# Performance work log

Measured on AMD Instinct MI355X. Metric: run time of the kernel, lower is better.

## Reference

```python
import jax, jax.numpy as jnp
import numpy as np

B, M, C = 8, 1024, 768


def setup_inputs() -> dict:
    key = jax.random.key(0)
    ks = jax.random.split(key, 10)
    s = 0.02
    return {
        "layout_x": jax.random.normal(ks[0], (B, M, C), jnp.float32),
        "text_x": jax.random.normal(ks[1], (B, M, C), jnp.float32),
        "mask": jax.random.randint(ks[2], (B, M), 0, 2).astype(jnp.float32),
        "Wqkv": jax.random.normal(ks[3], (C, 3 * C), jnp.float32) * s,
        "bqkv": jnp.zeros((3 * C,), jnp.float32),
        "Wq": jax.random.normal(ks[4], (C, C), jnp.float32) * s,
        "bq": jnp.zeros((C,), jnp.float32),
        "Wkv": jax.random.normal(ks[5], (C, 2 * C), jnp.float32) * s,
        "bkv": jnp.zeros((2 * C,), jnp.float32),
        "Wffn": jax.random.normal(ks[6], (C, C), jnp.float32) * s,
        "bffn": jnp.zeros((C,), jnp.float32),
    }


def _masked_attn(q, k, v, pair_mask, scale):
    # pair_mask: [B,M,M] True where valid (mask_i * mask_j != 0)
    scores = jnp.einsum("bmd,bnd->bmn", q, k) * scale  # [B,M,M]
    scores = jnp.where(pair_mask, scores, jnp.float32(-10000.0))
    attn = jax.nn.softmax(scores, axis=-1)
    return jnp.einsum("bmn,bnd->bmd", attn, v)


def reference(layout_x, text_x, mask, Wqkv, bqkv, Wq, bq, Wkv, bkv, Wffn, bffn):
    dim = layout_x.shape[-1]
    scale = dim ** (-0.5)
    # mask repeated over C then mask@mask.T / C  ==  outer product of 1D masks
    pair = (mask[:, :, None] * mask[:, None, :]) != 0  # [B,M,M] bool, True=keep

    # self-attention on layout_x
    qkv = layout_x @ Wqkv + bqkv  # [B,M,3C]
    q, k, v = jnp.split(qkv, 3, axis=-1)
    layout_o = _masked_attn(q, k, v, pair, scale)

    # cross-attention: q from layout output, k/v from text_x
    cq = layout_o @ Wq + bq
    kv = text_x @ Wkv + bkv  # [B,M,2C]
    ck, cv = jnp.split(kv, 2, axis=-1)
    merge = _masked_attn(cq, ck, cv, pair, scale)

    return merge @ Wffn + bffn
```

## Files before the change

kernel.cpp:

```cpp
#include <hip/hip_runtime.h>
#include <math.h>

#define BDIM 8
#define MDIM 1024
#define CDIM 768
#define ROWS (BDIM * MDIM)

typedef __attribute__((ext_vector_type(8))) short short8;
typedef __attribute__((ext_vector_type(8))) unsigned short ushort8;
typedef __attribute__((ext_vector_type(4))) float f32x4;

#define MFMA16(a, b, c) __builtin_amdgcn_mfma_f32_16x16x32_bf16((a), (b), (c), 0, 0, 0)

__device__ __forceinline__ unsigned short f2bf(float f) {
  unsigned u = __float_as_uint(f);
  return (unsigned short)((u + 0x7FFFu + ((u >> 16) & 1u)) >> 16);
}

__global__ __launch_bounds__(256) void convert_bf16(
    const float* __restrict__ src, unsigned short* __restrict__ dst, int n) {
  const int i = (blockIdx.x * 256 + threadIdx.x) * 8;
  if (i >= n) return;
  const float4 a = *(const float4*)(src + i);
  const float4 b = *(const float4*)(src + i + 4);
  ushort8 o;
  o[0] = f2bf(a.x); o[1] = f2bf(a.y); o[2] = f2bf(a.z); o[3] = f2bf(a.w);
  o[4] = f2bf(b.x); o[5] = f2bf(b.y); o[6] = f2bf(b.z); o[7] = f2bf(b.w);
  *(ushort8*)(dst + i) = o;
}

__global__ __launch_bounds__(256) void transpose_w(
    const float* __restrict__ W, int N, unsigned short* __restrict__ Wt) {
  __shared__ unsigned short t[32][33];
  const int tx = threadIdx.x, ty = threadIdx.y;
  const int n0 = blockIdx.x * 32, k0 = blockIdx.y * 32;
#pragma unroll
  for (int i = 0; i < 4; ++i)
    t[ty + i * 8][tx] = f2bf(W[(size_t)(k0 + ty + i * 8) * N + n0 + tx]);
  __syncthreads();
#pragma unroll
  for (int i = 0; i < 4; ++i)
    Wt[(size_t)(n0 + ty + i * 8) * CDIM + k0 + tx] = t[tx][ty + i * 8];
}

__global__ __launch_bounds__(256) void transpose_bf16(
    const unsigned short* __restrict__ src, int ld,
    unsigned short* __restrict__ dst) {
  __shared__ unsigned short t[32][33];
  const int tx = threadIdx.x, ty = threadIdx.y;
  const int n0 = blockIdx.x * 32, d0 = blockIdx.y * 32, b = blockIdx.z;
#pragma unroll
  for (int i = 0; i < 4; ++i) {
    const int n = n0 + ty + i * 8;
    t[ty + i * 8][tx] = src[(size_t)(b * MDIM + n) * ld + d0 + tx];
  }
  __syncthreads();
  unsigned short* db = dst + (size_t)b * CDIM * MDIM;
#pragma unroll
  for (int i = 0; i < 4; ++i) {
    const int d = d0 + ty + i * 8;
    db[(size_t)d * MDIM + n0 + tx] = t[tx][ty + i * 8];
  }
}

__device__ __forceinline__ void stage_tile(
    const unsigned short* __restrict__ g, int ld, int k0,
    unsigned short* lds, int wave, int lane) {
  const int gchunk = (lane & 3) ^ ((lane >> 3) & 3);
#pragma unroll
  for (int j = 0; j < 2; ++j) {
    const int grp = wave * 2 + j;
    const unsigned short* gp =
        g + (size_t)(grp * 16 + (lane >> 2)) * ld + k0 + gchunk * 8;
    __builtin_amdgcn_global_load_lds(
        (const __attribute__((address_space(1))) unsigned int*)gp,
        (__attribute__((address_space(3))) unsigned int*)(lds + grp * 512),
        16, 0, 0);
  }
}

__device__ __forceinline__ void mfma_loop(
    const unsigned short* __restrict__ A, int lda,
    const unsigned short* __restrict__ Bt, int ldb, int K,
    unsigned short* As, unsigned short* Bs, f32x4 acc[4][4],
    int wave, int lane) {
  const int wx = wave & 1, wy = wave >> 1;
  const int quad = lane >> 4, l16 = lane & 15;
  const int sq = (quad ^ ((l16 >> 1) & 3)) * 8;
  for (int k0 = 0; k0 < K; k0 += 32) {
    stage_tile(A, lda, k0, As, wave, lane);
    stage_tile(Bt, ldb, k0, Bs, wave, lane);
    __syncthreads();
    short8 afr[4], bfr[4];
#pragma unroll
    for (int mt = 0; mt < 4; ++mt)
      afr[mt] = *(const short8*)&As[(wy * 64 + mt * 16 + l16) * 32 + sq];
#pragma unroll
    for (int nt = 0; nt < 4; ++nt)
      bfr[nt] = *(const short8*)&Bs[(wx * 64 + nt * 16 + l16) * 32 + sq];
#pragma unroll
    for (int mt = 0; mt < 4; ++mt)
#pragma unroll
      for (int nt = 0; nt < 4; ++nt)
        acc[mt][nt] = MFMA16(afr[mt], bfr[nt], acc[mt][nt]);
    __syncthreads();
  }
}

template <bool BF16OUT>
__global__ __launch_bounds__(256, 3) void gemm_mfma(
    const unsigned short* __restrict__ A, const unsigned short* __restrict__ Bt,
    const float* __restrict__ bias, void* __restrict__ Yv) {
  __shared__ __align__(16) unsigned short As[128 * 32];
  __shared__ __align__(16) unsigned short Bs[128 * 32];
  const int c0 = blockIdx.x * 128;
  const int m0 = blockIdx.y * 128;
  const int tid = threadIdx.x;
  const int wave = tid >> 6, lane = tid & 63;
  const int wx = wave & 1, wy = wave >> 1;
  const int quad = lane >> 4, l16 = lane & 15;

  const f32x4 vzero = {0.f, 0.f, 0.f, 0.f};
  f32x4 acc[4][4];
#pragma unroll
  for (int mt = 0; mt < 4; ++mt)
#pragma unroll
    for (int nt = 0; nt < 4; ++nt) acc[mt][nt] = vzero;

  mfma_loop(A + (size_t)m0 * CDIM, CDIM, Bt + (size_t)c0 * CDIM, CDIM, CDIM,
            As, Bs, acc, wave, lane);

  const int slice = c0 / 768;
  const size_t sbase = (size_t)slice * ROWS * 768;
#pragma unroll
  for (int mt = 0; mt < 4; ++mt)
#pragma unroll
    for (int nt = 0; nt < 4; ++nt) {
      const int gcol = c0 + wx * 64 + nt * 16 + l16;
      const int lcol = gcol - slice * 768;
      const float bv = bias[gcol];
#pragma unroll
      for (int rg = 0; rg < 4; ++rg) {
        const int row = m0 + wy * 64 + mt * 16 + quad * 4 + rg;
        const float v = acc[mt][nt][rg] + bv;
        if (BF16OUT)
          ((unsigned short*)Yv)[sbase + (size_t)row * 768 + lcol] = f2bf(v);
        else
          ((float*)Yv)[sbase + (size_t)row * 768 + lcol] = v;
      }
    }
}

__global__ __launch_bounds__(256, 3) void gemm_qk(
    const unsigned short* __restrict__ Qb, const unsigned short* __restrict__ Kb,
    const float* __restrict__ mask, unsigned short* __restrict__ S, float scale) {
  __shared__ __align__(16) unsigned short As[128 * 32];
  __shared__ __align__(16) unsigned short Bs[128 * 32];
  const int c0 = blockIdx.x * 128;
  const int m0 = blockIdx.y * 128;
  const int b = blockIdx.z;
  const int tid = threadIdx.x;
  const int wave = tid >> 6, lane = tid & 63;
  const int wx = wave & 1, wy = wave >> 1;
  const int quad = lane >> 4, l16 = lane & 15;

  const f32x4 vzero = {0.f, 0.f, 0.f, 0.f};
  f32x4 acc[4][4];
#pragma unroll
  for (int mt = 0; mt < 4; ++mt)
#pragma unroll
    for (int nt = 0; nt < 4; ++nt) acc[mt][nt] = vzero;

  mfma_loop(Qb + ((size_t)b * MDIM + m0) * CDIM, CDIM,
            Kb + ((size_t)b * MDIM + c0) * CDIM, CDIM, CDIM,
            As, Bs, acc, wave, lane);

  const float* maskb = mask + b * MDIM;
  float mrow[4][4];
#pragma unroll
  for (int mt = 0; mt < 4; ++mt)
#pragma unroll
    for (int rg = 0; rg < 4; ++rg)
      mrow[mt][rg] = maskb[m0 + wy * 64 + mt * 16 + quad * 4 + rg];
  unsigned short* Sb = S + (size_t)b * MDIM * MDIM;
#pragma unroll
  for (int nt = 0; nt < 4; ++nt) {
    const int col = c0 + wx * 64 + nt * 16 + l16;
    const float mcol = maskb[col];
#pragma unroll
    for (int mt = 0; mt < 4; ++mt)
#pragma unroll
      for (int rg = 0; rg < 4; ++rg) {
        const int row = m0 + wy * 64 + mt * 16 + quad * 4 + rg;
        const float sv =
            (mrow[mt][rg] * mcol != 0.f) ? acc[mt][nt][rg] * scale : -10000.0f;
        Sb[(size_t)row * MDIM + col] = f2bf(sv);
      }
  }
}

__global__ __launch_bounds__(256) void softmax_row(unsigned short* __restrict__ S) {
  __shared__ float red[2][4];
  unsigned short* p = S + (size_t)blockIdx.x * MDIM;
  const int t = threadIdx.x;
  const int wave = t >> 6, lane = t & 63;
  const uint2 u = *(const uint2*)(p + t * 4);
  const float v0 = __uint_as_float((u.x & 0xFFFFu) << 16);
  const float v1 = __uint_as_float(u.x & 0xFFFF0000u);
  const float v2 = __uint_as_float((u.y & 0xFFFFu) << 16);
  const float v3 = __uint_as_float(u.y & 0xFFFF0000u);
  float mx = fmaxf(fmaxf(v0, v1), fmaxf(v2, v3));
  for (int off = 1; off < 64; off <<= 1) mx = fmaxf(mx, __shfl_xor(mx, off, 64));
  if (lane == 0) red[0][wave] = mx;
  __syncthreads();
  mx = fmaxf(fmaxf(red[0][0], red[0][1]), fmaxf(red[0][2], red[0][3]));
  const float e0 = __expf(v0 - mx), e1 = __expf(v1 - mx);
  const float e2 = __expf(v2 - mx), e3 = __expf(v3 - mx);
  float s = e0 + e1 + e2 + e3;
  for (int off = 1; off < 64; off <<= 1) s += __shfl_xor(s, off, 64);
  if (lane == 0) red[1][wave] = s;
  __syncthreads();
  const float inv = 1.f / (red[1][0] + red[1][1] + red[1][2] + red[1][3]);
  uint2 o;
  o.x = (unsigned)f2bf(e0 * inv) | ((unsigned)f2bf(e1 * inv) << 16);
  o.y = (unsigned)f2bf(e2 * inv) | ((unsigned)f2bf(e3 * inv) << 16);
  *(uint2*)(p + t * 4) = o;
}

__global__ __launch_bounds__(256, 3) void attn_pv(
    const unsigned short* __restrict__ P, const unsigned short* __restrict__ vT,
    unsigned short* __restrict__ O) {
  __shared__ __align__(16) unsigned short As[128 * 32];
  __shared__ __align__(16) unsigned short Bs[128 * 32];
  const int c0 = blockIdx.x * 128;
  const int m0 = blockIdx.y * 128;
  const int b = blockIdx.z;
  const int tid = threadIdx.x;
  const int wave = tid >> 6, lane = tid & 63;
  const int wx = wave & 1, wy = wave >> 1;
  const int quad = lane >> 4, l16 = lane & 15;

  const f32x4 vzero = {0.f, 0.f, 0.f, 0.f};
  f32x4 acc[4][4];
#pragma unroll
  for (int mt = 0; mt < 4; ++mt)
#pragma unroll
    for (int nt = 0; nt < 4; ++nt) acc[mt][nt] = vzero;

  mfma_loop(P + ((size_t)b * MDIM + m0) * MDIM, MDIM,
            vT + ((size_t)b * CDIM + c0) * MDIM, MDIM, MDIM,
            As, Bs, acc, wave, lane);

#pragma unroll
  for (int mt = 0; mt < 4; ++mt)
#pragma unroll
    for (int nt = 0; nt < 4; ++nt)
#pragma unroll
      for (int rg = 0; rg < 4; ++rg) {
        const int row = m0 + wy * 64 + mt * 16 + quad * 4 + rg;
        const int col = c0 + wx * 64 + nt * 16 + l16;
        O[(size_t)(b * MDIM + row) * CDIM + col] = f2bf(acc[mt][nt][rg]);
      }
}

extern "C" void kernel_launch(void* const* d_in, const int* in_sizes, int n_in,
                              void* d_out, int out_size, void* d_ws, size_t ws_size,
                              hipStream_t stream) {
  const float* layout_x = (const float*)d_in[0];
  const float* text_x   = (const float*)d_in[1];
  const float* maskp    = (const float*)d_in[2];
  const float* Wqkv     = (const float*)d_in[3];
  const float* bqkv     = (const float*)d_in[4];
  const float* Wq       = (const float*)d_in[5];
  const float* bq       = (const float*)d_in[6];
  const float* Wkv      = (const float*)d_in[7];
  const float* bkv      = (const float*)d_in[8];
  const float* Wffn     = (const float*)d_in[9];
  const float* bffn     = (const float*)d_in[10];
  float* out = (float*)d_out;
  char* ws = (char*)d_ws;

  const float scale = 1.0f / sqrtf((float)CDIM);

  unsigned short* xlb    = (unsigned short*)(ws);
  unsigned short* xtb    = (unsigned short*)(ws + 12582912);
  unsigned short* Wqkv_t = (unsigned short*)(ws + 25165824);
  unsigned short* Wq_t   = (unsigned short*)(ws + 28704768);
  unsigned short* Wkv_t  = (unsigned short*)(ws + 29884416);
  unsigned short* Wffn_t = (unsigned short*)(ws + 32243712);
  unsigned short* Qb     = (unsigned short*)(ws + 33423360);
  unsigned short* Kb     = (unsigned short*)(ws + 46006272);
  unsigned short* Vb     = (unsigned short*)(ws + 58589184);
  unsigned short* vT     = (unsigned short*)(ws + 71172096);
  unsigned short* S      = (unsigned short*)(ws + 83755008);
  unsigned short* attn1  = xlb;
  unsigned short* cqb    = Vb;
  unsigned short* Kc     = Qb;
  unsigned short* Vc     = Kb;

  convert_bf16<<<ROWS * CDIM / 2048, 256, 0, stream>>>(layout_x, xlb, ROWS * CDIM);
  convert_bf16<<<ROWS * CDIM / 2048, 256, 0, stream>>>(text_x, xtb, ROWS * CDIM);
  transpose_w<<<dim3(72, 24), dim3(32, 8), 0, stream>>>(Wqkv, 2304, Wqkv_t);
  transpose_w<<<dim3(24, 24), dim3(32, 8), 0, stream>>>(Wq, 768, Wq_t);
  transpose_w<<<dim3(48, 24), dim3(32, 8), 0, stream>>>(Wkv, 1536, Wkv_t);
  transpose_w<<<dim3(24, 24), dim3(32, 8), 0, stream>>>(Wffn, 768, Wffn_t);

  gemm_mfma<true><<<dim3(18, 64), 256, 0, stream>>>(xlb, Wqkv_t, bqkv, Qb);
  transpose_bf16<<<dim3(32, 24, BDIM), dim3(32, 8), 0, stream>>>(Vb, 768, vT);
  gemm_qk<<<dim3(8, 8, BDIM), 256, 0, stream>>>(Qb, Kb, maskp, S, scale);
  softmax_row<<<ROWS, 256, 0, stream>>>(S);
  attn_pv<<<dim3(6, 8, BDIM), 256, 0, stream>>>(S, vT, attn1);
  gemm_mfma<true><<<dim3(6, 64), 256, 0, stream>>>(attn1, Wq_t, bq, cqb);
  gemm_mfma<true><<<dim3(12, 64), 256, 0, stream>>>(xtb, Wkv_t, bkv, Kc);
  transpose_bf16<<<dim3(32, 24, BDIM), dim3(32, 8), 0, stream>>>(Vc, 768, vT);
  gemm_qk<<<dim3(8, 8, BDIM), 256, 0, stream>>>(cqb, Kc, maskp, S, scale);
  softmax_row<<<ROWS, 256, 0, stream>>>(S);
  attn_pv<<<dim3(6, 8, BDIM), 256, 0, stream>>>(S, vT, attn1);
  gemm_mfma<false><<<dim3(6, 64), 256, 0, stream>>>(attn1, Wffn_t, bffn, out);
}
```

Baseline: 379.5 us.

## Fuse V transpose into projection epilogue, double K tile, merge prep kernels

The V-slice of the QKV and KV projection GEMMs now writes its output directly in transposed layout, which removes the two standalone transpose_bf16 kernels and their extra pass over V. The GEMM mainloop stages 64-wide K tiles with a new XOR swizzle, halving the number of barrier pairs per K loop at the cost of doubling LDS per block. The input conversions and the four weight transposes are each merged into a single launch to cut launch overhead. The transposed epilogue writes 8-byte column strips, which may coalesce worse than the row-major stores, and the larger LDS footprint may limit occupancy.

```diff
diff --git a/kernel.cpp b/kernel.cpp
--- a/kernel.cpp
+++ b/kernel.cpp
@@ -17,8 +17,11 @@
   return (unsigned short)((u + 0x7FFFu + ((u >> 16) & 1u)) >> 16);
 }
 
-__global__ __launch_bounds__(256) void convert_bf16(
-    const float* __restrict__ src, unsigned short* __restrict__ dst, int n) {
+__global__ __launch_bounds__(256) void convert2_bf16(
+    const float* __restrict__ s0, const float* __restrict__ s1,
+    unsigned short* __restrict__ d0, unsigned short* __restrict__ d1, int n) {
+  const float* src = blockIdx.y ? s1 : s0;
+  unsigned short* dst = blockIdx.y ? d1 : d0;
   const int i = (blockIdx.x * 256 + threadIdx.x) * 8;
   if (i >= n) return;
   const float4 a = *(const float4*)(src + i);
@@ -29,49 +32,38 @@
   *(ushort8*)(dst + i) = o;
 }
 
-__global__ __launch_bounds__(256) void transpose_w(
-    const float* __restrict__ W, int N, unsigned short* __restrict__ Wt) {
+__global__ __launch_bounds__(256) void transpose_w_all(
+    const float* __restrict__ W0, const float* __restrict__ W1,
+    const float* __restrict__ W2, const float* __restrict__ W3,
+    unsigned short* __restrict__ D0, unsigned short* __restrict__ D1,
+    unsigned short* __restrict__ D2, unsigned short* __restrict__ D3) {
+  int x = blockIdx.x;
+  const float* W; unsigned short* D; int N;
+  if (x < 72)       { W = W0; D = D0; N = 2304; }
+  else if (x < 96)  { W = W1; D = D1; N = 768;  x -= 72; }
+  else if (x < 144) { W = W2; D = D2; N = 1536; x -= 96; }
+  else              { W = W3; D = D3; N = 768;  x -= 144; }
   __shared__ unsigned short t[32][33];
   const int tx = threadIdx.x, ty = threadIdx.y;
-  const int n0 = blockIdx.x * 32, k0 = blockIdx.y * 32;
+  const int n0 = x * 32, k0 = blockIdx.y * 32;
 #pragma unroll
   for (int i = 0; i < 4; ++i)
     t[ty + i * 8][tx] = f2bf(W[(size_t)(k0 + ty + i * 8) * N + n0 + tx]);
   __syncthreads();
 #pragma unroll
   for (int i = 0; i < 4; ++i)
-    Wt[(size_t)(n0 + ty + i * 8) * CDIM + k0 + tx] = t[tx][ty + i * 8];
-}
-
-__global__ __launch_bounds__(256) void transpose_bf16(
-    const unsigned short* __restrict__ src, int ld,
-    unsigned short* __restrict__ dst) {
-  __shared__ unsigned short t[32][33];
-  const int tx = threadIdx.x, ty = threadIdx.y;
-  const int n0 = blockIdx.x * 32, d0 = blockIdx.y * 32, b = blockIdx.z;
-#pragma unroll
-  for (int i = 0; i < 4; ++i) {
-    const int n = n0 + ty + i * 8;
-    t[ty + i * 8][tx] = src[(size_t)(b * MDIM + n) * ld + d0 + tx];
-  }
-  __syncthreads();
-  unsigned short* db = dst + (size_t)b * CDIM * MDIM;
-#pragma unroll
-  for (int i = 0; i < 4; ++i) {
-    const int d = d0 + ty + i * 8;
-    db[(size_t)d * MDIM + n0 + tx] = t[tx][ty + i * 8];
-  }
-}
-
-__device__ __forceinline__ void stage_tile(
+    D[(size_t)(n0 + ty + i * 8) * CDIM + k0 + tx] = t[tx][ty + i * 8];
+}
+
+__device__ __forceinline__ void stage64(
     const unsigned short* __restrict__ g, int ld, int k0,
     unsigned short* lds, int wave, int lane) {
-  const int gchunk = (lane & 3) ^ ((lane >> 3) & 3);
-#pragma unroll
-  for (int j = 0; j < 2; ++j) {
-    const int grp = wave * 2 + j;
+  const int gchunk = (lane & 7) ^ (lane >> 3);
+#pragma unroll
+  for (int j = 0; j < 4; ++j) {
+    const int grp = wave * 4 + j;
     const unsigned short* gp =
-        g + (size_t)(grp * 16 + (lane >> 2)) * ld + k0 + gchunk * 8;
+        g + (size_t)(grp * 8 + (lane >> 3)) * ld + k0 + gchunk * 8;
     __builtin_amdgcn_global_load_lds(
         (const __attribute__((address_space(1))) unsigned int*)gp,
         (__attribute__((address_space(3))) unsigned int*)(lds + grp * 512),
@@ -79,40 +71,44 @@
   }
 }
 
-__device__ __forceinline__ void mfma_loop(
+__device__ __forceinline__ void mfma_loop64(
     const unsigned short* __restrict__ A, int lda,
     const unsigned short* __restrict__ Bt, int ldb, int K,
     unsigned short* As, unsigned short* Bs, f32x4 acc[4][4],
     int wave, int lane) {
   const int wx = wave & 1, wy = wave >> 1;
   const int quad = lane >> 4, l16 = lane & 15;
-  const int sq = (quad ^ ((l16 >> 1) & 3)) * 8;
-  for (int k0 = 0; k0 < K; k0 += 32) {
-    stage_tile(A, lda, k0, As, wave, lane);
-    stage_tile(Bt, ldb, k0, Bs, wave, lane);
+  for (int k0 = 0; k0 < K; k0 += 64) {
+    stage64(A, lda, k0, As, wave, lane);
+    stage64(Bt, ldb, k0, Bs, wave, lane);
     __syncthreads();
-    short8 afr[4], bfr[4];
-#pragma unroll
-    for (int mt = 0; mt < 4; ++mt)
-      afr[mt] = *(const short8*)&As[(wy * 64 + mt * 16 + l16) * 32 + sq];
-#pragma unroll
-    for (int nt = 0; nt < 4; ++nt)
-      bfr[nt] = *(const short8*)&Bs[(wx * 64 + nt * 16 + l16) * 32 + sq];
-#pragma unroll
-    for (int mt = 0; mt < 4; ++mt)
+#pragma unroll
+    for (int h = 0; h < 2; ++h) {
+      const int slot = ((((h << 2) | quad) ^ (l16 & 7))) * 8;
+      short8 afr[4], bfr[4];
+#pragma unroll
+      for (int mt = 0; mt < 4; ++mt)
+        afr[mt] = *(const short8*)&As[(wy * 64 + mt * 16 + l16) * 64 + slot];
 #pragma unroll
       for (int nt = 0; nt < 4; ++nt)
-        acc[mt][nt] = MFMA16(afr[mt], bfr[nt], acc[mt][nt]);
+        bfr[nt] = *(const short8*)&Bs[(wx * 64 + nt * 16 + l16) * 64 + slot];
+#pragma unroll
+      for (int mt = 0; mt < 4; ++mt)
+#pragma unroll
+        for (int nt = 0; nt < 4; ++nt)
+          acc[mt][nt] = MFMA16(afr[mt], bfr[nt], acc[mt][nt]);
+    }
     __syncthreads();
   }
 }
 
-template <bool BF16OUT>
+template <bool BF16OUT, bool TRANS_LAST>
 __global__ __launch_bounds__(256, 3) void gemm_mfma(
     const unsigned short* __restrict__ A, const unsigned short* __restrict__ Bt,
-    const float* __restrict__ bias, void* __restrict__ Yv) {
-  __shared__ __align__(16) unsigned short As[128 * 32];
-  __shared__ __align__(16) unsigned short Bs[128 * 32];
+    const float* __restrict__ bias, void* __restrict__ Yv,
+    unsigned short* __restrict__ vTdst) {
+  __shared__ __align__(16) unsigned short As[128 * 64];
+  __shared__ __align__(16) unsigned short Bs[128 * 64];
   const int c0 = blockIdx.x * 128;
   const int m0 = blockIdx.y * 128;
   const int tid = threadIdx.x;
@@ -127,35 +123,55 @@
 #pragma unroll
     for (int nt = 0; nt < 4; ++nt) acc[mt][nt] = vzero;
 
-  mfma_loop(A + (size_t)m0 * CDIM, CDIM, Bt + (size_t)c0 * CDIM, CDIM, CDIM,
-            As, Bs, acc, wave, lane);
+  mfma_loop64(A + (size_t)m0 * CDIM, CDIM, Bt + (size_t)c0 * CDIM, CDIM, CDIM,
+              As, Bs, acc, wave, lane);
 
   const int slice = c0 / 768;
-  const size_t sbase = (size_t)slice * ROWS * 768;
-#pragma unroll
-  for (int mt = 0; mt < 4; ++mt)
-#pragma unroll
-    for (int nt = 0; nt < 4; ++nt) {
-      const int gcol = c0 + wx * 64 + nt * 16 + l16;
-      const int lcol = gcol - slice * 768;
-      const float bv = bias[gcol];
-#pragma unroll
-      for (int rg = 0; rg < 4; ++rg) {
-        const int row = m0 + wy * 64 + mt * 16 + quad * 4 + rg;
-        const float v = acc[mt][nt][rg] + bv;
-        if (BF16OUT)
-          ((unsigned short*)Yv)[sbase + (size_t)row * 768 + lcol] = f2bf(v);
-        else
-          ((float*)Yv)[sbase + (size_t)row * 768 + lcol] = v;
+  if (TRANS_LAST && slice == (int)(gridDim.x / 6) - 1) {
+#pragma unroll
+    for (int mt = 0; mt < 4; ++mt) {
+      const int row0 = m0 + wy * 64 + mt * 16 + quad * 4;
+      const int b = row0 >> 10, n0 = row0 & 1023;
+#pragma unroll
+      for (int nt = 0; nt < 4; ++nt) {
+        const int gcol = c0 + wx * 64 + nt * 16 + l16;
+        const int d = gcol - slice * 768;
+        const float bv = bias[gcol];
+        uint2 o;
+        o.x = (unsigned)f2bf(acc[mt][nt][0] + bv) |
+              ((unsigned)f2bf(acc[mt][nt][1] + bv) << 16);
+        o.y = (unsigned)f2bf(acc[mt][nt][2] + bv) |
+              ((unsigned)f2bf(acc[mt][nt][3] + bv) << 16);
+        *(uint2*)&vTdst[((size_t)b * CDIM + d) * MDIM + n0] = o;
       }
     }
+  } else {
+    const size_t sbase = (size_t)slice * ROWS * 768;
+#pragma unroll
+    for (int mt = 0; mt < 4; ++mt)
+#pragma unroll
+      for (int nt = 0; nt < 4; ++nt) {
+        const int gcol = c0 + wx * 64 + nt * 16 + l16;
+        const int lcol = gcol - slice * 768;
+        const float bv = bias[gcol];
+#pragma unroll
+        for (int rg = 0; rg < 4; ++rg) {
+          const int row = m0 + wy * 64 + mt * 16 + quad * 4 + rg;
+          const float v = acc[mt][nt][rg] + bv;
+          if (BF16OUT)
+            ((unsigned short*)Yv)[sbase + (size_t)row * 768 + lcol] = f2bf(v);
+          else
+            ((float*)Yv)[sbase + (size_t)row * 768 + lcol] = v;
+        }
+      }
+  }
 }
 
 __global__ __launch_bounds__(256, 3) void gemm_qk(
     const unsigned short* __restrict__ Qb, const unsigned short* __restrict__ Kb,
     const float* __restrict__ mask, unsigned short* __restrict__ S, float scale) {
-  __shared__ __align__(16) unsigned short As[128 * 32];
-  __shared__ __align__(16) unsigned short Bs[128 * 32];
+  __shared__ __align__(16) unsigned short As[128 * 64];
+  __shared__ __align__(16) unsigned short Bs[128 * 64];
   const int c0 = blockIdx.x * 128;
   const int m0 = blockIdx.y * 128;
   const int b = blockIdx.z;
@@ -171,9 +187,9 @@
 #pragma unroll
     for (int nt = 0; nt < 4; ++nt) acc[mt][nt] = vzero;
 
-  mfma_loop(Qb + ((size_t)b * MDIM + m0) * CDIM, CDIM,
-            Kb + ((size_t)b * MDIM + c0) * CDIM, CDIM, CDIM,
-            As, Bs, acc, wave, lane);
+  mfma_loop64(Qb + ((size_t)b * MDIM + m0) * CDIM, CDIM,
+              Kb + ((size_t)b * MDIM + c0) * CDIM, CDIM, CDIM,
+              As, Bs, acc, wave, lane);
 
   const float* maskb = mask + b * MDIM;
   float mrow[4][4];
@@ -230,8 +246,8 @@
 __global__ __launch_bounds__(256, 3) void attn_pv(
     const unsigned short* __restrict__ P, const unsigned short* __restrict__ vT,
     unsigned short* __restrict__ O) {
-  __shared__ __align__(16) unsigned short As[128 * 32];
-  __shared__ __align__(16) unsigned short Bs[128 * 32];
+  __shared__ __align__(16) unsigned short As[128 * 64];
+  __shared__ __align__(16) unsigned short Bs[128 * 64];
   const int c0 = blockIdx.x * 128;
   const int m0 = blockIdx.y * 128;
   const int b = blockIdx.z;
@@ -247,9 +263,9 @@
 #pragma unroll
     for (int nt = 0; nt < 4; ++nt) acc[mt][nt] = vzero;
 
-  mfma_loop(P + ((size_t)b * MDIM + m0) * MDIM, MDIM,
-            vT + ((size_t)b * CDIM + c0) * MDIM, MDIM, MDIM,
-            As, Bs, acc, wave, lane);
+  mfma_loop64(P + ((size_t)b * MDIM + m0) * MDIM, MDIM,
+              vT + ((size_t)b * CDIM + c0) * MDIM, MDIM, MDIM,
+              As, Bs, acc, wave, lane);
 
 #pragma unroll
   for (int mt = 0; mt < 4; ++mt)
@@ -296,25 +312,24 @@
   unsigned short* attn1  = xlb;
   unsigned short* cqb    = Vb;
   unsigned short* Kc     = Qb;
-  unsigned short* Vc     = Kb;
-
-  convert_bf16<<<ROWS * CDIM / 2048, 256, 0, stream>>>(layout_x, xlb, ROWS * CDIM);
-  convert_bf16<<<ROWS * CDIM / 2048, 256, 0, stream>>>(text_x, xtb, ROWS * CDIM);
-  transpose_w<<<dim3(72, 24), dim3(32, 8), 0, stream>>>(Wqkv, 2304, Wqkv_t);
-  transpose_w<<<dim3(24, 24), dim3(32, 8), 0, stream>>>(Wq, 768, Wq_t);
-  transpose_w<<<dim3(48, 24), dim3(32, 8), 0, stream>>>(Wkv, 1536, Wkv_t);
-  transpose_w<<<dim3(24, 24), dim3(32, 8), 0, stream>>>(Wffn, 768, Wffn_t);
-
-  gemm_mfma<true><<<dim3(18, 64), 256, 0, stream>>>(xlb, Wqkv_t, bqkv, Qb);
-  transpose_bf16<<<dim3(32, 24, BDIM), dim3(32, 8), 0, stream>>>(Vb, 768, vT);
+
+  convert2_bf16<<<dim3(ROWS * CDIM / 2048, 2), 256, 0, stream>>>(
+      layout_x, text_x, xlb, xtb, ROWS * CDIM);
+  transpose_w_all<<<dim3(168, 24), dim3(32, 8), 0, stream>>>(
+      Wqkv, Wq, Wkv, Wffn, Wqkv_t, Wq_t, Wkv_t, Wffn_t);
+
+  gemm_mfma<true, true><<<dim3(18, 64), 256, 0, stream>>>(
+      xlb, Wqkv_t, bqkv, Qb, vT);
   gemm_qk<<<dim3(8, 8, BDIM), 256, 0, stream>>>(Qb, Kb, maskp, S, scale);
   softmax_row<<<ROWS, 256, 0, stream>>>(S);
   attn_pv<<<dim3(6, 8, BDIM), 256, 0, stream>>>(S, vT, attn1);
-  gemm_mfma<true><<<dim3(6, 64), 256, 0, stream>>>(attn1, Wq_t, bq, cqb);
-  gemm_mfma<true><<<dim3(12, 64), 256, 0, stream>>>(xtb, Wkv_t, bkv, Kc);
-  transpose_bf16<<<dim3(32, 24, BDIM), dim3(32, 8), 0, stream>>>(Vc, 768, vT);
+  gemm_mfma<true, false><<<dim3(6, 64), 256, 0, stream>>>(
+      attn1, Wq_t, bq, cqb, vT);
+  gemm_mfma<true, true><<<dim3(12, 64), 256, 0, stream>>>(
+      xtb, Wkv_t, bkv, Kc, vT);
   gemm_qk<<<dim3(8, 8, BDIM), 256, 0, stream>>>(cqb, Kc, maskp, S, scale);
   softmax_row<<<ROWS, 256, 0, stream>>>(S);
   attn_pv<<<dim3(6, 8, BDIM), 256, 0, stream>>>(S, vT, attn1);
-  gemm_mfma<false><<<dim3(6, 64), 256, 0, stream>>>(attn1, Wffn_t, bffn, out);
-}
+  gemm_mfma<false, false><<<dim3(6, 64), 256, 0, stream>>>(
+      attn1, Wffn_t, bffn, out, vT);
+}
```

Result: faster. 338.4 us (-10.8%).
